# Optimization experiments

Hardware: AMD Instinct MI355X
Metric: run time of the kernel (lower is better)

## Reference

```python
import jax, jax.numpy as jnp
import numpy as np

FP8_MAX = 448.0  # max representable magnitude of float8_e4m3fn


def act_quant(x, block_size):
    """Blockwise fp8 quantization along the last dim.
    x: [M, K] -> q: [M, K//bs, bs] fp8, scale: [M, K//bs, 1] fp32."""
    m, k = x.shape
    xb = x.reshape(m, k // block_size, block_size)
    amax = jnp.max(jnp.abs(xb), axis=-1, keepdims=True)
    scale = jnp.maximum(amax, 1e-4) / FP8_MAX
    q = (xb / scale).astype(jnp.float8_e4m3fn)
    return q, scale


def dequant(q, scale):
    # q: [M, K//bs, bs], scale: [M, K//bs, 1] -> [M, K] fp32
    return (q.astype(jnp.float32) * scale).reshape(q.shape[0], -1)


def setup_inputs() -> dict:
    key = jax.random.key(0)
    k1, k2 = jax.random.split(key)
    B, S, D, F = 16, 4096, 512, 512
    x = jax.random.normal(k1, (B, S, D), dtype=jnp.float32)
    # lecun_normal-style init: std = 1/sqrt(fan_in)
    kernel = jax.random.normal(k2, (D, F), dtype=jnp.float32) / np.sqrt(D)
    bias = jnp.zeros((F,), dtype=jnp.float32)
    return {"x": x, "kernel": kernel, "bias": bias, "block_size": 128}


def reference(x, kernel, bias, block_size):
    input_shape = x.shape
    x_flat = x.reshape(-1, input_shape[-1])  # [M, K]
    # blockwise fp8 quantize activations and kernel
    xq, xs = act_quant(x_flat, block_size)
    kq, ks = act_quant(kernel, block_size)
    # fp8 GEMM with dequant scales == dequant-then-matmul in exact math
    y = dequant(xq, xs) @ dequant(kq, ks)  # [M, F]
    y = y + bias
    return y.reshape(input_shape[:-1] + (kernel.shape[1],))
```

## Files before the change

### kernel.cpp

```cpp
#include <hip/hip_runtime.h>
#include <hip/hip_bf16.h>

typedef __attribute__((ext_vector_type(4))) float  floatx4;
typedef __attribute__((ext_vector_type(2))) float  floatx2;
typedef __attribute__((ext_vector_type(8))) __bf16 bf16x8;

#define FP8_MAX 448.0f

__device__ __forceinline__ floatx2 fp8_qdq2(float a, float b) {
    int p = __builtin_amdgcn_cvt_pk_fp8_f32(a, b, 0, false);
    return __builtin_amdgcn_cvt_pk_f32_fp8(p, false);
}

__device__ __forceinline__ unsigned int f2bf(float f) {
    union { __hip_bfloat16 h; unsigned short u; } cv;
    cv.h = __float2bfloat16(f);
    return (unsigned int)cv.u;
}

__device__ __forceinline__ void async_copy16(void* lds, const void* g) {
    __builtin_amdgcn_global_load_lds(
        (const __attribute__((address_space(1))) unsigned int*)g,
        (__attribute__((address_space(3))) unsigned int*)lds, 16, 0, 0);
}

__global__ void wdq_kernel(const float* __restrict__ W,
                           __hip_bfloat16* __restrict__ Wt) {
    const int D = 512, F = 512;
    int d = blockIdx.x;
    int t = threadIdx.x;
    float4 v = *reinterpret_cast<const float4*>(W + (size_t)d * F + t * 4);
    float am = fmaxf(fmaxf(fabsf(v.x), fabsf(v.y)), fmaxf(fabsf(v.z), fabsf(v.w)));
#pragma unroll
    for (int s = 16; s >= 1; s >>= 1) am = fmaxf(am, __shfl_xor(am, s));
    float scale = fmaxf(am, 1e-4f) / FP8_MAX;
    floatx2 d01 = fp8_qdq2(v.x / scale, v.y / scale);
    floatx2 d23 = fp8_qdq2(v.z / scale, v.w / scale);
    int f0 = t * 4;
    Wt[(size_t)(f0 + 0) * D + d] = __float2bfloat16(d01[0] * scale);
    Wt[(size_t)(f0 + 1) * D + d] = __float2bfloat16(d01[1] * scale);
    Wt[(size_t)(f0 + 2) * D + d] = __float2bfloat16(d23[0] * scale);
    Wt[(size_t)(f0 + 3) * D + d] = __float2bfloat16(d23[1] * scale);
}

__global__ void xqdq_kernel(const float* __restrict__ X,
                            __hip_bfloat16* __restrict__ Xdq) {
    int tid = threadIdx.x;
    size_t row = (size_t)blockIdx.x * 2 + (tid >> 7);
    int cg = tid & 127;
    const float4 v = *reinterpret_cast<const float4*>(X + row * 512 + cg * 4);
    float am = fmaxf(fmaxf(fabsf(v.x), fabsf(v.y)), fmaxf(fabsf(v.z), fabsf(v.w)));
    am = fmaxf(am, __shfl_xor(am, 1));
    am = fmaxf(am, __shfl_xor(am, 2));
    am = fmaxf(am, __shfl_xor(am, 4));
    am = fmaxf(am, __shfl_xor(am, 8));
    am = fmaxf(am, __shfl_xor(am, 16));
    am = fmaxf(am, 1e-4f);
    float scale = am / FP8_MAX;
    float inv   = FP8_MAX / am;
    floatx2 d01 = fp8_qdq2(v.x * inv, v.y * inv);
    floatx2 d23 = fp8_qdq2(v.z * inv, v.w * inv);
    uint2 o;
    o.x = f2bf(d01[0] * scale) | (f2bf(d01[1] * scale) << 16);
    o.y = f2bf(d23[0] * scale) | (f2bf(d23[1] * scale) << 16);
    *reinterpret_cast<uint2*>(Xdq + row * 512 + cg * 4) = o;
}

__global__ __launch_bounds__(256, 2) void gemm8(
        const __hip_bfloat16* __restrict__ Xdq,
        const __hip_bfloat16* __restrict__ Wt,
        const float* __restrict__ bias,
        float* __restrict__ C, int M) {
    const int K = 512, N = 512;
    __shared__ char Abuf[2][16384];
    __shared__ char Bbuf[3][16384];

    int bx   = blockIdx.x;
    int tile = (bx & 7) * (gridDim.x >> 3) + (bx >> 3);
    int tn   = tile & 3;
    int tm   = tile >> 2;

    int tid = threadIdx.x, wid = tid >> 6, lane = tid & 63;
    int wm = wid >> 1, wn = wid & 1;
    int lr = lane & 15, lg = lane >> 4;

    const char* Abase = (const char*)(Xdq + (size_t)tm * 128 * K);
    const char* Bbase = (const char*)(Wt + (size_t)tn * 128 * K);
    float* Cb = C + (size_t)tm * 128 * N + tn * 128;

    floatx4 acc[4][4] = {};

    auto stageA = [&](int buf, int t) {
        int kb = t * 128;
#pragma unroll
        for (int i = 0; i < 4; ++i) {
            int c = wid * 4 + i;
            int r = c * 8 + (lane >> 3);
            int s = lane & 7;
            async_copy16(Abuf[buf] + c * 1024,
                         Abase + (size_t)r * 1024 + kb + ((s ^ (r & 7)) << 4));
        }
    };
    auto stageB = [&](int buf, int t) {
        int kb = t * 128;
#pragma unroll
        for (int i = 0; i < 4; ++i) {
            int c = wid * 4 + i;
            int f = c * 8 + (lane >> 3);
            int s = lane & 7;
            async_copy16(Bbuf[buf] + c * 1024,
                         Bbase + (size_t)f * 1024 + kb + ((s ^ (f & 7)) << 4));
        }
    };

    float bv[4];
#pragma unroll
    for (int ni = 0; ni < 4; ++ni)
        bv[ni] = bias[tn * 128 + wn * 64 + ni * 16 + lr];
    stageA(0, 0);
    stageB(0, 0);
    stageB(1, 1);
    asm volatile("s_waitcnt vmcnt(4)" ::: "memory");
    __builtin_amdgcn_s_barrier();
    __builtin_amdgcn_sched_barrier(0);

#pragma unroll
    for (int t = 0; t < 8; ++t) {
        const char* Ab = Abuf[t & 1];
        const char* Bb = Bbuf[t % 3];
        if (t < 7) stageA((t + 1) & 1, t + 1);
        if (t < 6) stageB((t + 2) % 3, t + 2);
        __builtin_amdgcn_s_setprio(1);
#pragma unroll
        for (int ks = 0; ks < 2; ++ks) {
            int q = (ks << 2) | lg;
            bf16x8 a[4], b[4];
#pragma unroll
            for (int mi = 0; mi < 4; ++mi) {
                int r = wm * 64 + mi * 16 + lr;
                a[mi] = *reinterpret_cast<const bf16x8*>(
                    Ab + r * 128 + ((q ^ (r & 7)) << 4));
            }
#pragma unroll
            for (int ni = 0; ni < 4; ++ni) {
                int f = wn * 64 + ni * 16 + lr;
                b[ni] = *reinterpret_cast<const bf16x8*>(
                    Bb + f * 128 + ((q ^ (f & 7)) << 4));
            }
#pragma unroll
            for (int mi = 0; mi < 4; ++mi)
#pragma unroll
                for (int ni = 0; ni < 4; ++ni)
                    acc[mi][ni] = __builtin_amdgcn_mfma_f32_16x16x32_bf16(
                        a[mi], b[ni], acc[mi][ni], 0, 0, 0);
        }
        __builtin_amdgcn_s_setprio(0);
        if (t < 7) {
            if (t < 6) asm volatile("s_waitcnt vmcnt(4)" ::: "memory");
            else       asm volatile("s_waitcnt vmcnt(0)" ::: "memory");
            __builtin_amdgcn_s_barrier();
            __builtin_amdgcn_sched_barrier(0);
        }
    }

#pragma unroll
    for (int ni = 0; ni < 4; ++ni) {
        int col = wn * 64 + ni * 16 + lr;
#pragma unroll
        for (int mi = 0; mi < 4; ++mi) {
            int r0 = wm * 64 + mi * 16 + lg * 4;
#pragma unroll
            for (int e = 0; e < 4; ++e)
                Cb[(size_t)(r0 + e) * N + col] = acc[mi][ni][e] + bv[ni];
        }
    }
}

extern "C" void kernel_launch(void* const* d_in, const int* in_sizes, int n_in,
                              void* d_out, int out_size, void* d_ws, size_t ws_size,
                              hipStream_t stream) {
    const float* X    = (const float*)d_in[0];
    const float* W    = (const float*)d_in[1];
    const float* bias = (const float*)d_in[2];
    const int K = 512;
    const int M = in_sizes[0] / K;

    __hip_bfloat16* Wt  = (__hip_bfloat16*)d_ws;
    __hip_bfloat16* Xdq = Wt + 512 * 512;

    wdq_kernel<<<dim3(512), dim3(128), 0, stream>>>(W, Wt);
    xqdq_kernel<<<dim3(M / 2), dim3(256), 0, stream>>>(X, Xdq);
    gemm8<<<dim3((M / 128) * (512 / 128)), dim3(256), 0, stream>>>(
        Xdq, Wt, bias, (float*)d_out, M);
}
```

Measured before the change: 96.88 us.

## Load GEMM B operand straight to registers and widen the activation quant kernel

The GEMM no longer stages the weight tile through LDS. Each wave loads its B fragments straight from global memory into double-buffered registers, while A keeps a three-deep LDS ring and the occupancy hint goes from 2 to 3 blocks per CU. The activation quantize-dequantize kernel now handles 8 elements per thread and 4 rows per block, with 16-byte stores. The aim is to cut LDS traffic and footprint so more blocks fit per CU, at the cost of more registers and uncoalesced, unswizzled global B reads that rely on cache hits.

```diff
diff --git a/kernel.cpp b/kernel.cpp
--- a/kernel.cpp
+++ b/kernel.cpp
@@ -46,34 +46,41 @@
 __global__ void xqdq_kernel(const float* __restrict__ X,
                             __hip_bfloat16* __restrict__ Xdq) {
     int tid = threadIdx.x;
-    size_t row = (size_t)blockIdx.x * 2 + (tid >> 7);
-    int cg = tid & 127;
-    const float4 v = *reinterpret_cast<const float4*>(X + row * 512 + cg * 4);
-    float am = fmaxf(fmaxf(fabsf(v.x), fabsf(v.y)), fmaxf(fabsf(v.z), fabsf(v.w)));
+    size_t row = (size_t)blockIdx.x * 4 + (tid >> 6);
+    int lane = tid & 63;
+    const float* src = X + row * 512 + lane * 8;
+    float4 v0 = *reinterpret_cast<const float4*>(src);
+    float4 v1 = *reinterpret_cast<const float4*>(src + 4);
+    float am = fmaxf(fmaxf(fmaxf(fabsf(v0.x), fabsf(v0.y)),
+                           fmaxf(fabsf(v0.z), fabsf(v0.w))),
+                     fmaxf(fmaxf(fabsf(v1.x), fabsf(v1.y)),
+                           fmaxf(fabsf(v1.z), fabsf(v1.w))));
     am = fmaxf(am, __shfl_xor(am, 1));
     am = fmaxf(am, __shfl_xor(am, 2));
     am = fmaxf(am, __shfl_xor(am, 4));
     am = fmaxf(am, __shfl_xor(am, 8));
-    am = fmaxf(am, __shfl_xor(am, 16));
     am = fmaxf(am, 1e-4f);
     float scale = am / FP8_MAX;
     float inv   = FP8_MAX / am;
-    floatx2 d01 = fp8_qdq2(v.x * inv, v.y * inv);
-    floatx2 d23 = fp8_qdq2(v.z * inv, v.w * inv);
-    uint2 o;
-    o.x = f2bf(d01[0] * scale) | (f2bf(d01[1] * scale) << 16);
-    o.y = f2bf(d23[0] * scale) | (f2bf(d23[1] * scale) << 16);
-    *reinterpret_cast<uint2*>(Xdq + row * 512 + cg * 4) = o;
-}
-
-__global__ __launch_bounds__(256, 2) void gemm8(
+    floatx2 a0 = fp8_qdq2(v0.x * inv, v0.y * inv);
+    floatx2 a1 = fp8_qdq2(v0.z * inv, v0.w * inv);
+    floatx2 a2 = fp8_qdq2(v1.x * inv, v1.y * inv);
+    floatx2 a3 = fp8_qdq2(v1.z * inv, v1.w * inv);
+    uint4 o;
+    o.x = f2bf(a0[0] * scale) | (f2bf(a0[1] * scale) << 16);
+    o.y = f2bf(a1[0] * scale) | (f2bf(a1[1] * scale) << 16);
+    o.z = f2bf(a2[0] * scale) | (f2bf(a2[1] * scale) << 16);
+    o.w = f2bf(a3[0] * scale) | (f2bf(a3[1] * scale) << 16);
+    *reinterpret_cast<uint4*>(Xdq + row * 512 + lane * 8) = o;
+}
+
+__global__ __launch_bounds__(256, 3) void gemm9(
         const __hip_bfloat16* __restrict__ Xdq,
         const __hip_bfloat16* __restrict__ Wt,
         const float* __restrict__ bias,
         float* __restrict__ C, int M) {
     const int K = 512, N = 512;
-    __shared__ char Abuf[2][16384];
-    __shared__ char Bbuf[3][16384];
+    __shared__ char Abuf[3][16384];
 
     int bx   = blockIdx.x;
     int tile = (bx & 7) * (gridDim.x >> 3) + (bx >> 3);
@@ -89,6 +96,7 @@
     float* Cb = C + (size_t)tm * 128 * N + tn * 128;
 
     floatx4 acc[4][4] = {};
+    bf16x8 bA[8], bB[8];
 
     auto stageA = [&](int buf, int t) {
         int kb = t * 128;
@@ -101,40 +109,22 @@
                          Abase + (size_t)r * 1024 + kb + ((s ^ (r & 7)) << 4));
         }
     };
-    auto stageB = [&](int buf, int t) {
-        int kb = t * 128;
-#pragma unroll
-        for (int i = 0; i < 4; ++i) {
-            int c = wid * 4 + i;
-            int f = c * 8 + (lane >> 3);
-            int s = lane & 7;
-            async_copy16(Bbuf[buf] + c * 1024,
-                         Bbase + (size_t)f * 1024 + kb + ((s ^ (f & 7)) << 4));
-        }
+    auto loadB = [&](bf16x8* b, int t) {
+#pragma unroll
+        for (int ks = 0; ks < 2; ++ks)
+#pragma unroll
+            for (int ni = 0; ni < 4; ++ni) {
+                int f = wn * 64 + ni * 16 + lr;
+                int q = ks * 4 + lg;
+                b[ks * 4 + ni] = *reinterpret_cast<const bf16x8*>(
+                    Bbase + (size_t)f * 1024 + t * 128 + q * 16);
+            }
     };
-
-    float bv[4];
-#pragma unroll
-    for (int ni = 0; ni < 4; ++ni)
-        bv[ni] = bias[tn * 128 + wn * 64 + ni * 16 + lr];
-    stageA(0, 0);
-    stageB(0, 0);
-    stageB(1, 1);
-    asm volatile("s_waitcnt vmcnt(4)" ::: "memory");
-    __builtin_amdgcn_s_barrier();
-    __builtin_amdgcn_sched_barrier(0);
-
-#pragma unroll
-    for (int t = 0; t < 8; ++t) {
-        const char* Ab = Abuf[t & 1];
-        const char* Bb = Bbuf[t % 3];
-        if (t < 7) stageA((t + 1) & 1, t + 1);
-        if (t < 6) stageB((t + 2) % 3, t + 2);
-        __builtin_amdgcn_s_setprio(1);
+    auto mfmaStep = [&](const char* Ab, const bf16x8* b) {
 #pragma unroll
         for (int ks = 0; ks < 2; ++ks) {
             int q = (ks << 2) | lg;
-            bf16x8 a[4], b[4];
+            bf16x8 a[4];
 #pragma unroll
             for (int mi = 0; mi < 4; ++mi) {
                 int r = wm * 64 + mi * 16 + lr;
@@ -142,22 +132,38 @@
                     Ab + r * 128 + ((q ^ (r & 7)) << 4));
             }
 #pragma unroll
-            for (int ni = 0; ni < 4; ++ni) {
-                int f = wn * 64 + ni * 16 + lr;
-                b[ni] = *reinterpret_cast<const bf16x8*>(
-                    Bb + f * 128 + ((q ^ (f & 7)) << 4));
-            }
-#pragma unroll
             for (int mi = 0; mi < 4; ++mi)
 #pragma unroll
                 for (int ni = 0; ni < 4; ++ni)
                     acc[mi][ni] = __builtin_amdgcn_mfma_f32_16x16x32_bf16(
-                        a[mi], b[ni], acc[mi][ni], 0, 0, 0);
-        }
+                        a[mi], b[ks * 4 + ni], acc[mi][ni], 0, 0, 0);
+        }
+    };
+
+    float bv[4];
+#pragma unroll
+    for (int ni = 0; ni < 4; ++ni)
+        bv[ni] = bias[tn * 128 + wn * 64 + ni * 16 + lr];
+    __builtin_amdgcn_sched_barrier(0);
+    stageA(0, 0);
+    stageA(1, 1);
+    __builtin_amdgcn_sched_barrier(0);
+    loadB(bA, 0);
+    __builtin_amdgcn_sched_barrier(0);
+    asm volatile("s_waitcnt vmcnt(12)" ::: "memory");
+    __builtin_amdgcn_s_barrier();
+    __builtin_amdgcn_sched_barrier(0);
+
+#pragma unroll
+    for (int t = 0; t < 8; ++t) {
+        if (t < 6) stageA((t + 2) % 3, t + 2);
+        if (t < 7) loadB((t & 1) ? bA : bB, t + 1);
+        __builtin_amdgcn_s_setprio(1);
+        mfmaStep(Abuf[t % 3], (t & 1) ? bB : bA);
         __builtin_amdgcn_s_setprio(0);
         if (t < 7) {
-            if (t < 6) asm volatile("s_waitcnt vmcnt(4)" ::: "memory");
-            else       asm volatile("s_waitcnt vmcnt(0)" ::: "memory");
+            if (t < 6) asm volatile("s_waitcnt vmcnt(12)" ::: "memory");
+            else       asm volatile("s_waitcnt vmcnt(8)"  ::: "memory");
             __builtin_amdgcn_s_barrier();
             __builtin_amdgcn_sched_barrier(0);
         }
@@ -189,7 +195,7 @@
     __hip_bfloat16* Xdq = Wt + 512 * 512;
 
     wdq_kernel<<<dim3(512), dim3(128), 0, stream>>>(W, Wt);
-    xqdq_kernel<<<dim3(M / 2), dim3(256), 0, stream>>>(X, Xdq);
-    gemm8<<<dim3((M / 128) * (512 / 128)), dim3(256), 0, stream>>>(
+    xqdq_kernel<<<dim3(M / 4), dim3(256), 0, stream>>>(X, Xdq);
+    gemm9<<<dim3((M / 128) * (512 / 128)), dim3(256), 0, stream>>>(
         Xdq, Wt, bias, (float*)d_out, M);
 }
```

Measured after the change: 121.6 us. 25.5% more time.
